# Optimization experiments

Measured on AMD Instinct MI355X. Metric: run time of the kernel, lower is better.

Reference implementation:

```python
import jax, jax.numpy as jnp
import numpy as np

D_OUT, D_IN, RANK = 4096, 4096, 512
BATCH, SEQ = 4, 2048


def setup_inputs() -> dict:
    key = jax.random.key(0)
    kx, ka, kb, kc = jax.random.split(key, 4)
    x = jax.random.normal(kx, (BATCH, SEQ, D_IN), dtype=jnp.float32)
    # CP/low-rank factors: weight = A @ B.T, shape [D_OUT, D_IN]
    A = jax.random.normal(ka, (D_OUT, RANK), dtype=jnp.float32) * (1.0 / np.sqrt(RANK))
    B = jax.random.normal(kb, (D_IN, RANK), dtype=jnp.float32) * (1.0 / np.sqrt(D_IN))
    bias = jax.random.normal(kc, (D_OUT,), dtype=jnp.float32)
    return {"x": x, "A": A, "B": B, "bias": bias}


def reference(x, A, B, bias):
    # method == 'cp_2d': reconstruct weight then apply F.linear
    weight = A @ B.T                      # [D_OUT, D_IN]
    # F.linear(x, W, b) = x @ W.T + b
    out = jnp.einsum('bsd,od->bso', x, weight) + bias
    return out
```

## Files before the change

kernel.cpp:

```cpp
#include <hip/hip_runtime.h>

typedef __attribute__((ext_vector_type(8))) __bf16 bf16x8;
typedef __attribute__((ext_vector_type(4))) __bf16 bf16x4;
typedef __attribute__((ext_vector_type(4))) float f32x4;

#define D_OUT 4096
#define D_IN  4096
#define RANK  512
#define MROWS 8192

__device__ __forceinline__ void gload_lds16(const void* gsrc, void* ldst) {
  __builtin_amdgcn_global_load_lds(
      (const __attribute__((address_space(1))) void*)gsrc,
      (__attribute__((address_space(3))) void*)ldst, 16, 0, 0);
}

__global__ __launch_bounds__(256) void cvt_f32_bf16(const float* __restrict__ in,
                                                    __bf16* __restrict__ out,
                                                    size_t n) {
  size_t i = ((size_t)blockIdx.x * 256 + threadIdx.x) * 4;
  size_t stride = (size_t)gridDim.x * 256 * 4;
  for (; i < n; i += stride) {
    float4 v = *(const float4*)(in + i);
    bf16x4 o = {(__bf16)v.x, (__bf16)v.y, (__bf16)v.z, (__bf16)v.w};
    *(bf16x4*)(out + i) = o;
  }
}

__global__ __launch_bounds__(256) void transpose_cvt(const float* __restrict__ in,
                                                     __bf16* __restrict__ out,
                                                     int R, int C) {
  __shared__ __bf16 tile[64][72];
  const int r0 = blockIdx.x * 64, c0 = blockIdx.y * 64;
  const int t = threadIdx.x;
  const int tr = t / 16, tc4 = (t % 16) * 4;
#pragma unroll
  for (int i = 0; i < 4; ++i) {
    int r = i * 16 + tr;
    float4 v = *(const float4*)(in + (size_t)(r0 + r) * C + c0 + tc4);
    tile[r][tc4 + 0] = (__bf16)v.x;
    tile[r][tc4 + 1] = (__bf16)v.y;
    tile[r][tc4 + 2] = (__bf16)v.z;
    tile[r][tc4 + 3] = (__bf16)v.w;
  }
  __syncthreads();
#pragma unroll
  for (int i = 0; i < 4; ++i) {
    int c = i * 16 + tr;
    bf16x4 o = {tile[tc4 + 0][c], tile[tc4 + 1][c], tile[tc4 + 2][c], tile[tc4 + 3][c]};
    *(bf16x4*)(out + (size_t)(c0 + c) * R + r0 + tc4) = o;
  }
}

__global__ __launch_bounds__(256) void reduce2_bf16(const __bf16* __restrict__ t0,
                                                    const __bf16* __restrict__ t1,
                                                    __bf16* __restrict__ o) {
  size_t i = ((size_t)blockIdx.x * 256 + threadIdx.x) * 8;
  bf16x8 a = *(const bf16x8*)(t0 + i);
  bf16x8 b = *(const bf16x8*)(t1 + i);
  bf16x8 r;
#pragma unroll
  for (int j = 0; j < 8; ++j) r[j] = (__bf16)((float)a[j] + (float)b[j]);
  *(bf16x8*)(o + i) = r;
}

template <int BM, int BN, int BK>
__global__ __launch_bounds__(256) void gemm1_xf32(const float* __restrict__ Xf,
                                                  const __bf16* __restrict__ Bmat,
                                                  __bf16* __restrict__ Cout,
                                                  int M, int N, int Kred, int ldk) {
  constexpr int WM = BM / 2, WN = BN / 2;
  constexpr int MI = WM / 16, NI = WN / 16;
  __shared__ alignas(16) float Af[BM * BK];
  __shared__ alignas(16) __bf16 Bl[BN * BK];

  const int tid = threadIdx.x;
  const int wid = tid >> 6;
  const int lane = tid & 63;
  const int l15 = lane & 15, lhi = lane >> 4;
  const int wr = wid >> 1, wc = wid & 1;

  const int m0 = blockIdx.x * BM;
  const int n0 = blockIdx.y * BN;
  const int kbase = blockIdx.z * Kred;

  f32x4 acc[MI][NI] = {};

  for (int k0 = kbase; k0 < kbase + Kred; k0 += BK) {
    constexpr int IAF = BM * BK / (256 * 4);
#pragma unroll
    for (int it = 0; it < IAF; ++it) {
      int o = (it * 256 + tid) * 4;
      int row = o / BK;
      int b = (o % BK) / 4;
      int colsw = (b ^ (row & 7)) * 4;
      gload_lds16(Xf + (size_t)(m0 + row) * ldk + k0 + colsw,
                  Af + (it * 256 + wid * 64) * 4);
    }
    constexpr int IB = BN * BK / (256 * 8);
#pragma unroll
    for (int it = 0; it < IB; ++it) {
      int o = (it * 256 + tid) * 8;
      int row = o / BK;
      int blk = (o % BK) / 8;
      int col = (blk ^ (row & 7)) * 8;
      gload_lds16(Bmat + (size_t)(n0 + row) * ldk + k0 + col,
                  Bl + (it * 256 + wid * 64) * 8);
    }
    __syncthreads();

#pragma unroll
    for (int kk = 0; kk < BK / 32; ++kk) {
      bf16x8 af[MI], bfv[NI];
#pragma unroll
      for (int mi = 0; mi < MI; ++mi) {
        int row = wr * WM + mi * 16 + l15;
        int b0 = (kk * 8 + lhi * 2) ^ (row & 7);
        const char* base = (const char*)Af + row * (BK * 4);
        f32x4 a0 = *(const f32x4*)(base + b0 * 16);
        f32x4 a1 = *(const f32x4*)(base + (b0 ^ 1) * 16);
#pragma unroll
        for (int j = 0; j < 4; ++j) {
          af[mi][j]     = (__bf16)a0[j];
          af[mi][4 + j] = (__bf16)a1[j];
        }
      }
#pragma unroll
      for (int ni = 0; ni < NI; ++ni) {
        int row = wc * WN + ni * 16 + l15;
        int blk = (kk * 4 + lhi) ^ (row & 7);
        bfv[ni] = *(const bf16x8*)((const char*)Bl + row * (BK * 2) + blk * 16);
      }
#pragma unroll
      for (int mi = 0; mi < MI; ++mi)
#pragma unroll
        for (int ni = 0; ni < NI; ++ni)
          acc[mi][ni] = __builtin_amdgcn_mfma_f32_16x16x32_bf16(af[mi], bfv[ni],
                                                                acc[mi][ni], 0, 0, 0);
    }
    __syncthreads();
  }

  __bf16* cbase = Cout + (size_t)blockIdx.z * M * N;
#pragma unroll
  for (int ni = 0; ni < NI; ++ni) {
    int col = n0 + wc * WN + ni * 16 + l15;
#pragma unroll
    for (int mi = 0; mi < MI; ++mi) {
#pragma unroll
      for (int r = 0; r < 4; ++r) {
        int row = m0 + wr * WM + mi * 16 + lhi * 4 + r;
        cbase[(size_t)row * N + col] = (__bf16)acc[mi][ni][r];
      }
    }
  }
}

template <int BM, int BN, int BK>
__global__ __launch_bounds__(256) void gemm2_dbuf(const __bf16* __restrict__ Amat,
                                                  const __bf16* __restrict__ Bmat,
                                                  const float* __restrict__ bias,
                                                  float* __restrict__ Cout,
                                                  int M, int N, int K) {
  constexpr int WM = BM / 2, WN = BN / 2;
  constexpr int MI = WM / 16, NI = WN / 16;
  __shared__ alignas(16) __bf16 Al[2][BM * BK];
  __shared__ alignas(16) __bf16 Bl[2][BN * BK];

  const int tid = threadIdx.x;
  const int wid = tid >> 6;
  const int lane = tid & 63;
  const int l15 = lane & 15, lhi = lane >> 4;
  const int wr = wid >> 1, wc = wid & 1;

  const int m0 = blockIdx.x * BM;
  const int n0 = blockIdx.y * BN;
  const int nt = K / BK;

  f32x4 acc[MI][NI] = {};

  auto stage = [&](int k0, int b) {
    constexpr int IA = BM * BK / (256 * 8);
#pragma unroll
    for (int it = 0; it < IA; ++it) {
      int o = (it * 256 + tid) * 8;
      int row = o / BK;
      int blk = (o % BK) / 8;
      int col = (blk ^ (row & 7)) * 8;
      gload_lds16(Amat + (size_t)(m0 + row) * K + k0 + col,
                  &Al[b][(it * 256 + wid * 64) * 8]);
    }
    constexpr int IB = BN * BK / (256 * 8);
#pragma unroll
    for (int it = 0; it < IB; ++it) {
      int o = (it * 256 + tid) * 8;
      int row = o / BK;
      int blk = (o % BK) / 8;
      int col = (blk ^ (row & 7)) * 8;
      gload_lds16(Bmat + (size_t)(n0 + row) * K + k0 + col,
                  &Bl[b][(it * 256 + wid * 64) * 8]);
    }
  };

  stage(0, 0);
  __syncthreads();

  for (int t = 0; t < nt; ++t) {
    if (t + 1 < nt) stage((t + 1) * BK, (t + 1) & 1);

    const char* Ab_ = (const char*)Al[t & 1];
    const char* Bb_ = (const char*)Bl[t & 1];
#pragma unroll
    for (int kk = 0; kk < BK / 32; ++kk) {
      bf16x8 af[MI], bfv[NI];
#pragma unroll
      for (int mi = 0; mi < MI; ++mi) {
        int row = wr * WM + mi * 16 + l15;
        int blk = (kk * 4 + lhi) ^ (row & 7);
        af[mi] = *(const bf16x8*)(Ab_ + row * (BK * 2) + blk * 16);
      }
#pragma unroll
      for (int ni = 0; ni < NI; ++ni) {
        int row = wc * WN + ni * 16 + l15;
        int blk = (kk * 4 + lhi) ^ (row & 7);
        bfv[ni] = *(const bf16x8*)(Bb_ + row * (BK * 2) + blk * 16);
      }
#pragma unroll
      for (int mi = 0; mi < MI; ++mi)
#pragma unroll
        for (int ni = 0; ni < NI; ++ni)
          acc[mi][ni] = __builtin_amdgcn_mfma_f32_16x16x32_bf16(af[mi], bfv[ni],
                                                                acc[mi][ni], 0, 0, 0);
    }
    __syncthreads();
  }

#pragma unroll
  for (int ni = 0; ni < NI; ++ni) {
    int col = n0 + wc * WN + ni * 16 + l15;
    float bv = bias[col];
#pragma unroll
    for (int mi = 0; mi < MI; ++mi) {
#pragma unroll
      for (int r = 0; r < 4; ++r) {
        int row = m0 + wr * WM + mi * 16 + lhi * 4 + r;
        Cout[(size_t)row * N + col] = acc[mi][ni][r] + bv;
      }
    }
  }
}

extern "C" void kernel_launch(void* const* d_in, const int* in_sizes, int n_in,
                              void* d_out, int out_size, void* d_ws, size_t ws_size,
                              hipStream_t stream) {
  const float* x    = (const float*)d_in[0];
  const float* A    = (const float*)d_in[1];
  const float* B    = (const float*)d_in[2];
  const float* bias = (const float*)d_in[3];
  float* out = (float*)d_out;

  __bf16* tp = (__bf16*)((char*)d_out + ((size_t)64 << 20));
  char* ws = (char*)d_ws;
  __bf16* Ab = (__bf16*)ws;
  __bf16* Bt = (__bf16*)(ws + ((size_t)4 << 20));
  __bf16* Tt = (__bf16*)(ws + ((size_t)8 << 20));

  hipLaunchKernelGGL(cvt_f32_bf16, dim3(512), dim3(256), 0, stream,
                     A, Ab, (size_t)D_OUT * RANK);
  hipLaunchKernelGGL(transpose_cvt, dim3(D_IN / 64, RANK / 64), dim3(256), 0, stream,
                     B, Bt, D_IN, RANK);
  hipLaunchKernelGGL((gemm1_xf32<128, 128, 64>),
                     dim3(MROWS / 128, RANK / 128, 2), dim3(256), 0, stream,
                     x, Bt, tp, MROWS, RANK, D_IN / 2, D_IN);
  hipLaunchKernelGGL(reduce2_bf16, dim3(MROWS * RANK / (256 * 8)), dim3(256), 0, stream,
                     tp, tp + (size_t)MROWS * RANK, Tt);
  hipLaunchKernelGGL((gemm2_dbuf<128, 128, 64>),
                     dim3(MROWS / 128, D_OUT / 128), dim3(256), 0, stream,
                     Tt, Ab, bias, out, MROWS, D_OUT, RANK);
}
```

Before: 147.4 us.

## Pre-convert x to bf16, double-buffer and swizzle gemm1, single-buffer gemm2

Adds a separate pass that converts x from fp32 to bf16 into scratch space inside the output buffer, so gemm1 stages bf16 tiles instead of fp32 tiles and no longer converts in its inner loop. gemm1 gains double-buffered LDS staging and a block-index swizzle to improve L2 locality. gemm2 goes back to single-buffered LDS, which lowers LDS use and may raise occupancy. The extra conversion pass reads the full 128MB x and writes 64MB of bf16, which adds memory traffic.

```diff
diff --git a/kernel.cpp b/kernel.cpp
--- a/kernel.cpp
+++ b/kernel.cpp
@@ -65,14 +65,14 @@
 }
 
 template <int BM, int BN, int BK>
-__global__ __launch_bounds__(256) void gemm1_xf32(const float* __restrict__ Xf,
-                                                  const __bf16* __restrict__ Bmat,
-                                                  __bf16* __restrict__ Cout,
-                                                  int M, int N, int Kred, int ldk) {
+__global__ __launch_bounds__(256) void gemm1_dbuf_swz(const __bf16* __restrict__ Amat,
+                                                      const __bf16* __restrict__ Bmat,
+                                                      __bf16* __restrict__ Cout,
+                                                      int M, int N, int Kred, int ldk) {
   constexpr int WM = BM / 2, WN = BN / 2;
   constexpr int MI = WM / 16, NI = WN / 16;
-  __shared__ alignas(16) float Af[BM * BK];
-  __shared__ alignas(16) __bf16 Bl[BN * BK];
+  __shared__ alignas(16) __bf16 Al[2][BM * BK];
+  __shared__ alignas(16) __bf16 Bl[2][BN * BK];
 
   const int tid = threadIdx.x;
   const int wid = tid >> 6;
@@ -80,22 +80,27 @@
   const int l15 = lane & 15, lhi = lane >> 4;
   const int wr = wid >> 1, wc = wid & 1;
 
-  const int m0 = blockIdx.x * BM;
-  const int n0 = blockIdx.y * BN;
+  const int gx = gridDim.x;
+  const int nwg = gx * gridDim.y;
+  const int bid = blockIdx.y * gx + blockIdx.x;
+  const int swz = (bid & 7) * (nwg >> 3) + (bid >> 3);
+  const int m0 = (swz % gx) * BM;
+  const int n0 = (swz / gx) * BN;
   const int kbase = blockIdx.z * Kred;
+  const int nt = Kred / BK;
 
   f32x4 acc[MI][NI] = {};
 
-  for (int k0 = kbase; k0 < kbase + Kred; k0 += BK) {
-    constexpr int IAF = BM * BK / (256 * 4);
-#pragma unroll
-    for (int it = 0; it < IAF; ++it) {
-      int o = (it * 256 + tid) * 4;
-      int row = o / BK;
-      int b = (o % BK) / 4;
-      int colsw = (b ^ (row & 7)) * 4;
-      gload_lds16(Xf + (size_t)(m0 + row) * ldk + k0 + colsw,
-                  Af + (it * 256 + wid * 64) * 4);
+  auto stage = [&](int k0, int b) {
+    constexpr int IA = BM * BK / (256 * 8);
+#pragma unroll
+    for (int it = 0; it < IA; ++it) {
+      int o = (it * 256 + tid) * 8;
+      int row = o / BK;
+      int blk = (o % BK) / 8;
+      int col = (blk ^ (row & 7)) * 8;
+      gload_lds16(Amat + (size_t)(m0 + row) * ldk + k0 + col,
+                  &Al[b][(it * 256 + wid * 64) * 8]);
     }
     constexpr int IB = BN * BK / (256 * 8);
 #pragma unroll
@@ -105,31 +110,32 @@
       int blk = (o % BK) / 8;
       int col = (blk ^ (row & 7)) * 8;
       gload_lds16(Bmat + (size_t)(n0 + row) * ldk + k0 + col,
-                  Bl + (it * 256 + wid * 64) * 8);
-    }
-    __syncthreads();
-
+                  &Bl[b][(it * 256 + wid * 64) * 8]);
+    }
+  };
+
+  stage(kbase, 0);
+  __syncthreads();
+
+  for (int t = 0; t < nt; ++t) {
+    if (t + 1 < nt) stage(kbase + (t + 1) * BK, (t + 1) & 1);
+
+    const char* Ab_ = (const char*)Al[t & 1];
+    const char* Bb_ = (const char*)Bl[t & 1];
 #pragma unroll
     for (int kk = 0; kk < BK / 32; ++kk) {
       bf16x8 af[MI], bfv[NI];
 #pragma unroll
       for (int mi = 0; mi < MI; ++mi) {
         int row = wr * WM + mi * 16 + l15;
-        int b0 = (kk * 8 + lhi * 2) ^ (row & 7);
-        const char* base = (const char*)Af + row * (BK * 4);
-        f32x4 a0 = *(const f32x4*)(base + b0 * 16);
-        f32x4 a1 = *(const f32x4*)(base + (b0 ^ 1) * 16);
-#pragma unroll
-        for (int j = 0; j < 4; ++j) {
-          af[mi][j]     = (__bf16)a0[j];
-          af[mi][4 + j] = (__bf16)a1[j];
-        }
+        int blk = (kk * 4 + lhi) ^ (row & 7);
+        af[mi] = *(const bf16x8*)(Ab_ + row * (BK * 2) + blk * 16);
       }
 #pragma unroll
       for (int ni = 0; ni < NI; ++ni) {
         int row = wc * WN + ni * 16 + l15;
         int blk = (kk * 4 + lhi) ^ (row & 7);
-        bfv[ni] = *(const bf16x8*)((const char*)Bl + row * (BK * 2) + blk * 16);
+        bfv[ni] = *(const bf16x8*)(Bb_ + row * (BK * 2) + blk * 16);
       }
 #pragma unroll
       for (int mi = 0; mi < MI; ++mi)
@@ -157,15 +163,15 @@
 }
 
 template <int BM, int BN, int BK>
-__global__ __launch_bounds__(256) void gemm2_dbuf(const __bf16* __restrict__ Amat,
-                                                  const __bf16* __restrict__ Bmat,
-                                                  const float* __restrict__ bias,
-                                                  float* __restrict__ Cout,
-                                                  int M, int N, int K) {
+__global__ __launch_bounds__(256) void gemm2_plain(const __bf16* __restrict__ Amat,
+                                                   const __bf16* __restrict__ Bmat,
+                                                   const float* __restrict__ bias,
+                                                   float* __restrict__ Cout,
+                                                   int M, int N, int K) {
   constexpr int WM = BM / 2, WN = BN / 2;
   constexpr int MI = WM / 16, NI = WN / 16;
-  __shared__ alignas(16) __bf16 Al[2][BM * BK];
-  __shared__ alignas(16) __bf16 Bl[2][BN * BK];
+  __shared__ alignas(16) __bf16 Al[BM * BK];
+  __shared__ alignas(16) __bf16 Bl[BN * BK];
 
   const int tid = threadIdx.x;
   const int wid = tid >> 6;
@@ -175,11 +181,10 @@
 
   const int m0 = blockIdx.x * BM;
   const int n0 = blockIdx.y * BN;
-  const int nt = K / BK;
 
   f32x4 acc[MI][NI] = {};
 
-  auto stage = [&](int k0, int b) {
+  for (int k0 = 0; k0 < K; k0 += BK) {
     constexpr int IA = BM * BK / (256 * 8);
 #pragma unroll
     for (int it = 0; it < IA; ++it) {
@@ -188,7 +193,7 @@
       int blk = (o % BK) / 8;
       int col = (blk ^ (row & 7)) * 8;
       gload_lds16(Amat + (size_t)(m0 + row) * K + k0 + col,
-                  &Al[b][(it * 256 + wid * 64) * 8]);
+                  Al + (it * 256 + wid * 64) * 8);
     }
     constexpr int IB = BN * BK / (256 * 8);
 #pragma unroll
@@ -198,18 +203,10 @@
       int blk = (o % BK) / 8;
       int col = (blk ^ (row & 7)) * 8;
       gload_lds16(Bmat + (size_t)(n0 + row) * K + k0 + col,
-                  &Bl[b][(it * 256 + wid * 64) * 8]);
-    }
-  };
-
-  stage(0, 0);
-  __syncthreads();
-
-  for (int t = 0; t < nt; ++t) {
-    if (t + 1 < nt) stage((t + 1) * BK, (t + 1) & 1);
-
-    const char* Ab_ = (const char*)Al[t & 1];
-    const char* Bb_ = (const char*)Bl[t & 1];
+                  Bl + (it * 256 + wid * 64) * 8);
+    }
+    __syncthreads();
+
 #pragma unroll
     for (int kk = 0; kk < BK / 32; ++kk) {
       bf16x8 af[MI], bfv[NI];
@@ -217,13 +214,13 @@
       for (int mi = 0; mi < MI; ++mi) {
         int row = wr * WM + mi * 16 + l15;
         int blk = (kk * 4 + lhi) ^ (row & 7);
-        af[mi] = *(const bf16x8*)(Ab_ + row * (BK * 2) + blk * 16);
+        af[mi] = *(const bf16x8*)((const char*)Al + row * (BK * 2) + blk * 16);
       }
 #pragma unroll
       for (int ni = 0; ni < NI; ++ni) {
         int row = wc * WN + ni * 16 + l15;
         int blk = (kk * 4 + lhi) ^ (row & 7);
-        bfv[ni] = *(const bf16x8*)(Bb_ + row * (BK * 2) + blk * 16);
+        bfv[ni] = *(const bf16x8*)((const char*)Bl + row * (BK * 2) + blk * 16);
       }
 #pragma unroll
       for (int mi = 0; mi < MI; ++mi)
@@ -259,22 +256,25 @@
   const float* bias = (const float*)d_in[3];
   float* out = (float*)d_out;
 
+  __bf16* xb = (__bf16*)d_out;
   __bf16* tp = (__bf16*)((char*)d_out + ((size_t)64 << 20));
   char* ws = (char*)d_ws;
   __bf16* Ab = (__bf16*)ws;
   __bf16* Bt = (__bf16*)(ws + ((size_t)4 << 20));
   __bf16* Tt = (__bf16*)(ws + ((size_t)8 << 20));
 
+  hipLaunchKernelGGL(cvt_f32_bf16, dim3(2048), dim3(256), 0, stream,
+                     x, xb, (size_t)MROWS * D_IN);
   hipLaunchKernelGGL(cvt_f32_bf16, dim3(512), dim3(256), 0, stream,
                      A, Ab, (size_t)D_OUT * RANK);
   hipLaunchKernelGGL(transpose_cvt, dim3(D_IN / 64, RANK / 64), dim3(256), 0, stream,
                      B, Bt, D_IN, RANK);
-  hipLaunchKernelGGL((gemm1_xf32<128, 128, 64>),
+  hipLaunchKernelGGL((gemm1_dbuf_swz<128, 128, 64>),
                      dim3(MROWS / 128, RANK / 128, 2), dim3(256), 0, stream,
-                     x, Bt, tp, MROWS, RANK, D_IN / 2, D_IN);
+                     xb, Bt, tp, MROWS, RANK, D_IN / 2, D_IN);
   hipLaunchKernelGGL(reduce2_bf16, dim3(MROWS * RANK / (256 * 8)), dim3(256), 0, stream,
                      tp, tp + (size_t)MROWS * RANK, Tt);
-  hipLaunchKernelGGL((gemm2_dbuf<128, 128, 64>),
+  hipLaunchKernelGGL((gemm2_plain<128, 128, 64>),
                      dim3(MROWS / 128, D_OUT / 128), dim3(256), 0, stream,
                      Tt, Ab, bias, out, MROWS, D_OUT, RANK);
 }
```

Result: no change. 149.0 us (+1.0%).
